# Kernel optimization log

Measured on AMD Instinct MI355X. Metric: run time of the kernel, lower is better.

Reference implementation:

```python
import jax, jax.numpy as jnp
import numpy as np

B, S, D = 8, 2048, 512
EPS = 1e-6
ROPE_THETA = 10000.0


def setup_inputs() -> dict:
    key = jax.random.key(0)
    ks = jax.random.split(key, 8)
    scale = 0.02
    return {
        "x": jax.random.normal(ks[0], (B, S, D), dtype=jnp.float32),
        "conv_w": jax.random.normal(ks[1], (D, D, 3), dtype=jnp.float32) * scale,
        "conv_b": jnp.zeros((D,), dtype=jnp.float32),
        "pre_g": jnp.ones((D,), dtype=jnp.float32),
        "q_g": jnp.ones((D,), dtype=jnp.float32),
        "k_g": jnp.ones((D,), dtype=jnp.float32),
        "Wq": jax.random.normal(ks[2], (D, D), dtype=jnp.float32) * scale,
        "Wk": jax.random.normal(ks[3], (D, D), dtype=jnp.float32) * scale,
        "Wv": jax.random.normal(ks[4], (D, D), dtype=jnp.float32) * scale,
    }


def _rmsnorm(x, g, eps=EPS):
    ms = jnp.mean(jnp.square(x), axis=-1, keepdims=True)
    return x * jax.lax.rsqrt(ms + eps) * g


def _rope_tables(seq_len, head_dim, dtype=jnp.float32):
    inv = 1.0 / (ROPE_THETA ** (jnp.arange(0, head_dim, 2, dtype=dtype) / head_dim))
    freqs = jnp.arange(seq_len, dtype=dtype)[:, None] * inv[None, :]  # [S, D/2]
    return jnp.cos(freqs), jnp.sin(freqs)


def _apply_rope(x, cos, sin):
    # x: [B, S, D]; treat last dim as D/2 complex pairs (interleaved real/imag)
    b, s, d = x.shape
    xr = x.reshape(b, s, d // 2, 2)
    x0, x1 = xr[..., 0], xr[..., 1]
    c = cos[None, :, :]
    sn = sin[None, :, :]
    o0 = x0 * c - x1 * sn
    o1 = x0 * sn + x1 * c
    return jnp.stack([o0, o1], axis=-1).reshape(b, s, d)


def reference(x, conv_w, conv_b, pre_g, q_g, k_g, Wq, Wk, Wv):
    b, s, d = x.shape
    # Conv1d over sequence axis (kernel 3, padding 1)
    xc = jnp.transpose(x, (0, 2, 1))  # [B, D, S]
    xc = jax.lax.conv_general_dilated(
        xc, conv_w, window_strides=(1,), padding=[(1, 1)],
        dimension_numbers=("NCH", "OIH", "NCH"))
    xc = xc + conv_b[None, :, None]
    x_norm = _rmsnorm(jnp.transpose(xc, (0, 2, 1)), pre_g)  # [B, S, D]

    q = _rmsnorm(jnp.einsum("bsd,ed->bse", x_norm, Wq), q_g)
    k = _rmsnorm(jnp.einsum("bsd,ed->bse", x_norm, Wk), k_g)
    v = jnp.einsum("bsd,ed->bse", x_norm, Wv)

    cos, sin = _rope_tables(s, d, x.dtype)
    q = _apply_rope(q, cos, sin)
    k = _apply_rope(k, cos, sin)

    scores = jnp.einsum("bqd,bkd->bqk", q, k) / jnp.sqrt(jnp.asarray(d, x.dtype))
    w = jax.nn.softmax(scores, axis=-1)  # dropout is identity in eval mode
    attended = jnp.einsum("bqk,bkd->bqd", w, v)
    out = x + attended
    return out.mean(axis=1)  # [B, D]
```

## Files before the change

### kernel.cpp

```cpp
#include <hip/hip_runtime.h>
#include <math.h>

#define BB 8
#define SS 2048
#define DDIM 512
#define KC 1536
#define EPSV 1e-6f
#define SCALE 0.044194173824159216f
#define LDP 40

typedef unsigned short ushort_t;
using short8 = __attribute__((ext_vector_type(8))) short;
using f32x4  = __attribute__((ext_vector_type(4))) float;

__device__ inline unsigned short f2bf(float f) {
    union { float f; unsigned int u; } v; v.f = f;
    unsigned int r = v.u + 0x7FFFu + ((v.u >> 16) & 1u);
    return (unsigned short)(r >> 16);
}
__device__ inline unsigned int packbf(float a, float b) {
    return (unsigned int)f2bf(a) | ((unsigned int)f2bf(b) << 16);
}
__device__ inline float bf2f(unsigned short s) {
    union { unsigned int u; float f; } v; v.u = ((unsigned int)s) << 16; return v.f;
}
__device__ inline short8 ldfrag(const ushort_t* s, int row, int ko) {
    return *reinterpret_cast<const short8*>(&s[row * LDP + ko]);
}

__global__ __launch_bounds__(256) void kx_cast(const float* __restrict__ x, ushort_t* __restrict__ xbf)
{
    int i = (blockIdx.x * 256 + threadIdx.x) * 4;
    float4 v = *reinterpret_cast<const float4*>(&x[i]);
    unsigned int lo = packbf(v.x, v.y), hi = packbf(v.z, v.w);
    *reinterpret_cast<uint2*>(&xbf[i]) = make_uint2(lo, hi);
}

__global__ __launch_bounds__(256) void k0_prep(
    const float* __restrict__ conv_w, const float* __restrict__ Wq,
    const float* __restrict__ Wk, const float* __restrict__ Wv,
    ushort_t* __restrict__ wcat, ushort_t* __restrict__ wqkv)
{
    int idx = blockIdx.x * 256 + threadIdx.x;
    {
        int o = idx / KC, kk = idx - o * KC;
        int t = kk >> 9, i = kk & 511;
        wcat[idx] = f2bf(conv_w[(size_t)o * KC + i * 3 + t]);
    }
    {
        int n = idx >> 9, d = idx & 511;
        const float* src = (n < 512) ? &Wq[(size_t)n * DDIM + d]
                         : (n < 1024) ? &Wk[(size_t)(n - 512) * DDIM + d]
                         : &Wv[(size_t)(n - 1024) * DDIM + d];
        wqkv[idx] = f2bf(*src);
    }
}

__global__ __launch_bounds__(256, 4) void k1b_conv(
    const ushort_t* __restrict__ xbf, const ushort_t* __restrict__ wcat,
    const float* __restrict__ conv_b, float* __restrict__ y, float* __restrict__ rs)
{
    __shared__ ushort_t As[128 * LDP];
    __shared__ ushort_t Bs[128 * LDP];
    const int t = threadIdx.x;
    const int lane = t & 63, w = t >> 6;
    const int lm = lane & 15, lq = lane >> 4;
    const int wm = w >> 1, wn = w & 1;
    const int srow = t >> 2, scol = (t & 3) * 8;
    const int s0 = blockIdx.x * 128;
    const int n0 = blockIdx.y * 128;
    const int b  = blockIdx.z;
    const ushort_t* Ag = xbf + (size_t)b * SS * DDIM;
    const ushort_t* Bg = wcat + (size_t)n0 * KC;

    f32x4 acc[4][4];
    #pragma unroll
    for (int i = 0; i < 4; i++)
        #pragma unroll
        for (int j = 0; j < 4; j++) acc[i][j] = (f32x4){0.f, 0.f, 0.f, 0.f};

    const uint4 z4 = make_uint4(0, 0, 0, 0);
    #define LOADA(dc, ro, dst) { \
        int s_ = s0 + srow + (ro) + ((dc) >> 4) - 1; \
        int ic_ = (((dc) & 15) << 5) + scol; \
        dst = (s_ >= 0 && s_ < SS) ? *reinterpret_cast<const uint4*>(&Ag[(size_t)s_ * DDIM + ic_]) : z4; }

    uint4 ra0, ra1, rb0, rb1;
    LOADA(0, 0, ra0); LOADA(0, 64, ra1);
    rb0 = *reinterpret_cast<const uint4*>(&Bg[(size_t)srow * KC + scol]);
    rb1 = *reinterpret_cast<const uint4*>(&Bg[(size_t)(srow + 64) * KC + scol]);

    for (int dc = 0; dc < 48; dc++) {
        *reinterpret_cast<uint4*>(&As[srow * LDP + scol]) = ra0;
        *reinterpret_cast<uint4*>(&As[(srow + 64) * LDP + scol]) = ra1;
        *reinterpret_cast<uint4*>(&Bs[srow * LDP + scol]) = rb0;
        *reinterpret_cast<uint4*>(&Bs[(srow + 64) * LDP + scol]) = rb1;
        __syncthreads();
        if (dc < 47) {
            LOADA(dc + 1, 0, ra0); LOADA(dc + 1, 64, ra1);
            int c = (dc + 1) * 32 + scol;
            rb0 = *reinterpret_cast<const uint4*>(&Bg[(size_t)srow * KC + c]);
            rb1 = *reinterpret_cast<const uint4*>(&Bg[(size_t)(srow + 64) * KC + c]);
        }
        short8 af[4];
        #pragma unroll
        for (int mt = 0; mt < 4; mt++)
            af[mt] = ldfrag(As, wm * 64 + mt * 16 + lm, lq * 8);
        #pragma unroll
        for (int nt = 0; nt < 4; nt++) {
            short8 bfv = ldfrag(Bs, wn * 64 + nt * 16 + lm, lq * 8);
            #pragma unroll
            for (int mt = 0; mt < 4; mt++)
                acc[mt][nt] = __builtin_amdgcn_mfma_f32_16x16x32_bf16(af[mt], bfv, acc[mt][nt], 0, 0, 0);
        }
        __syncthreads();
    }
    #undef LOADA

    const int rbase = s0 + wm * 64;
    const int cbase = n0 + wn * 64;
    float* yb  = y + (size_t)b * SS * DDIM;
    float* rsb = rs + (size_t)b * SS;
    float bias[4];
    #pragma unroll
    for (int nt = 0; nt < 4; nt++) bias[nt] = conv_b[cbase + nt * 16 + lm];
    #pragma unroll
    for (int mt = 0; mt < 4; mt++) {
        float pr[4] = {0.f, 0.f, 0.f, 0.f};
        #pragma unroll
        for (int nt = 0; nt < 4; nt++) {
            #pragma unroll
            for (int r = 0; r < 4; r++) {
                float val = acc[mt][nt][r] + bias[nt];
                yb[(size_t)(rbase + mt * 16 + lq * 4 + r) * DDIM + cbase + nt * 16 + lm] = val;
                pr[r] = fmaf(val, val, pr[r]);
            }
        }
        #pragma unroll
        for (int r = 0; r < 4; r++) {
            float p = pr[r];
            p += __shfl_xor(p, 1, 64); p += __shfl_xor(p, 2, 64);
            p += __shfl_xor(p, 4, 64); p += __shfl_xor(p, 8, 64);
            if (lm == 0) atomicAdd(&rsb[rbase + mt * 16 + lq * 4 + r], p);
        }
    }
}

__global__ __launch_bounds__(256) void k1n_norm(
    const float* __restrict__ y, const float* __restrict__ rs,
    const float* __restrict__ pre_g, ushort_t* __restrict__ xnbf)
{
    const int t = threadIdx.x;
    const int b = blockIdx.y;
    const int r0 = blockIdx.x * 8;
    float2 pg = *reinterpret_cast<const float2*>(&pre_g[2 * t]);
    for (int r = 0; r < 8; r++) {
        size_t row = (size_t)b * SS + r0 + r;
        float inv = rsqrtf(rs[row] * (1.0f / DDIM) + EPSV);
        float2 v = *reinterpret_cast<const float2*>(&y[row * DDIM + 2 * t]);
        *reinterpret_cast<unsigned int*>(&xnbf[row * DDIM + 2 * t]) =
            packbf(v.x * inv * pg.x, v.y * inv * pg.y);
    }
}

__global__ __launch_bounds__(256, 4) void k1c_qkv(
    const ushort_t* __restrict__ xnbf, const ushort_t* __restrict__ wqkv,
    float* __restrict__ qraw, float* __restrict__ kraw, ushort_t* __restrict__ vb,
    float* __restrict__ rq, float* __restrict__ rk)
{
    __shared__ ushort_t As[128 * LDP];
    __shared__ ushort_t Bs[128 * LDP];
    const int t = threadIdx.x;
    const int lane = t & 63, w = t >> 6;
    const int lm = lane & 15, lq = lane >> 4;
    const int wm = w >> 1, wn = w & 1;
    const int srow = t >> 2, scol = (t & 3) * 8;
    const int s0 = blockIdx.x * 128;
    const int n0 = blockIdx.y * 128;
    const int b  = blockIdx.z;
    const ushort_t* Ag = xnbf + (size_t)b * SS * DDIM;
    const ushort_t* Bg = wqkv + (size_t)n0 * DDIM;

    f32x4 acc[4][4];
    #pragma unroll
    for (int i = 0; i < 4; i++)
        #pragma unroll
        for (int j = 0; j < 4; j++) acc[i][j] = (f32x4){0.f, 0.f, 0.f, 0.f};

    uint4 ra0 = *reinterpret_cast<const uint4*>(&Ag[(size_t)(s0 + srow) * DDIM + scol]);
    uint4 ra1 = *reinterpret_cast<const uint4*>(&Ag[(size_t)(s0 + srow + 64) * DDIM + scol]);
    uint4 rb0 = *reinterpret_cast<const uint4*>(&Bg[(size_t)srow * DDIM + scol]);
    uint4 rb1 = *reinterpret_cast<const uint4*>(&Bg[(size_t)(srow + 64) * DDIM + scol]);

    for (int dc = 0; dc < 16; dc++) {
        *reinterpret_cast<uint4*>(&As[srow * LDP + scol]) = ra0;
        *reinterpret_cast<uint4*>(&As[(srow + 64) * LDP + scol]) = ra1;
        *reinterpret_cast<uint4*>(&Bs[srow * LDP + scol]) = rb0;
        *reinterpret_cast<uint4*>(&Bs[(srow + 64) * LDP + scol]) = rb1;
        __syncthreads();
        if (dc < 15) {
            int c = (dc + 1) * 32 + scol;
            ra0 = *reinterpret_cast<const uint4*>(&Ag[(size_t)(s0 + srow) * DDIM + c]);
            ra1 = *reinterpret_cast<const uint4*>(&Ag[(size_t)(s0 + srow + 64) * DDIM + c]);
            rb0 = *reinterpret_cast<const uint4*>(&Bg[(size_t)srow * DDIM + c]);
            rb1 = *reinterpret_cast<const uint4*>(&Bg[(size_t)(srow + 64) * DDIM + c]);
        }
        short8 af[4];
        #pragma unroll
        for (int mt = 0; mt < 4; mt++)
            af[mt] = ldfrag(As, wm * 64 + mt * 16 + lm, lq * 8);
        #pragma unroll
        for (int nt = 0; nt < 4; nt++) {
            short8 bfv = ldfrag(Bs, wn * 64 + nt * 16 + lm, lq * 8);
            #pragma unroll
            for (int mt = 0; mt < 4; mt++)
                acc[mt][nt] = __builtin_amdgcn_mfma_f32_16x16x32_bf16(af[mt], bfv, acc[mt][nt], 0, 0, 0);
        }
        __syncthreads();
    }

    const int which = blockIdx.y >> 2;
    const int rbase = s0 + wm * 64;
    const int cbase = ((blockIdx.y & 3) * 128) + wn * 64;
    if (which == 2) {
        ushort_t* vbb = vb + (size_t)b * SS * DDIM;
        #pragma unroll
        for (int mt = 0; mt < 4; mt++)
            #pragma unroll
            for (int nt = 0; nt < 4; nt++)
                #pragma unroll
                for (int r = 0; r < 4; r++)
                    vbb[(size_t)(rbase + mt * 16 + lq * 4 + r) * DDIM + cbase + nt * 16 + lm] =
                        f2bf(acc[mt][nt][r]);
    } else {
        float* dst = which ? kraw : qraw;
        float* rr  = which ? rk : rq;
        float* db  = dst + (size_t)b * SS * DDIM;
        float* rb  = rr + (size_t)b * SS;
        #pragma unroll
        for (int mt = 0; mt < 4; mt++) {
            float pr[4] = {0.f, 0.f, 0.f, 0.f};
            #pragma unroll
            for (int nt = 0; nt < 4; nt++) {
                #pragma unroll
                for (int r = 0; r < 4; r++) {
                    float val = acc[mt][nt][r];
                    db[(size_t)(rbase + mt * 16 + lq * 4 + r) * DDIM + cbase + nt * 16 + lm] = val;
                    pr[r] = fmaf(val, val, pr[r]);
                }
            }
            #pragma unroll
            for (int r = 0; r < 4; r++) {
                float p = pr[r];
                p += __shfl_xor(p, 1, 64); p += __shfl_xor(p, 2, 64);
                p += __shfl_xor(p, 4, 64); p += __shfl_xor(p, 8, 64);
                if (lm == 0) atomicAdd(&rb[rbase + mt * 16 + lq * 4 + r], p);
            }
        }
    }
}

__global__ __launch_bounds__(256) void k1d_rope(
    const float* __restrict__ qraw, const float* __restrict__ kraw,
    const float* __restrict__ rq, const float* __restrict__ rk,
    const float* __restrict__ q_g, const float* __restrict__ k_g,
    ushort_t* __restrict__ qb, ushort_t* __restrict__ kb)
{
    const int t = threadIdx.x;
    const int b = blockIdx.y;
    const int r0 = blockIdx.x * 8;
    const int c0 = 2 * t;
    float qg0 = q_g[c0], qg1 = q_g[c0 + 1];
    float kg0 = k_g[c0], kg1 = k_g[c0 + 1];
    float invf = (float)pow(10000.0, -(double)c0 / (double)DDIM);
    for (int r = 0; r < 8; r++) {
        int srow = r0 + r;
        size_t rowi = (size_t)b * SS + srow;
        float iq = rsqrtf(rq[rowi] * (1.0f / DDIM) + EPSV);
        float ik = rsqrtf(rk[rowi] * (1.0f / DDIM) + EPSV);
        size_t off = rowi * DDIM + c0;
        float2 qv = *reinterpret_cast<const float2*>(&qraw[off]);
        float2 kv = *reinterpret_cast<const float2*>(&kraw[off]);
        float q0 = qv.x * iq * qg0, q1 = qv.y * iq * qg1;
        float k0v = kv.x * ik * kg0, k1v = kv.y * ik * kg1;
        float ang = (float)srow * invf, sn, cs;
        sincosf(ang, &sn, &cs);
        *reinterpret_cast<unsigned int*>(&qb[off]) = packbf(q0 * cs - q1 * sn, q0 * sn + q1 * cs);
        *reinterpret_cast<unsigned int*>(&kb[off]) = packbf(k0v * cs - k1v * sn, k0v * sn + k1v * cs);
    }
}

__global__ __launch_bounds__(256, 4) void k2a_rowsum(
    const ushort_t* __restrict__ qb, const ushort_t* __restrict__ kb,
    ushort_t* __restrict__ P, float* __restrict__ l)
{
    __shared__ ushort_t As[128 * LDP];
    __shared__ ushort_t Bs[128 * LDP];
    const int t = threadIdx.x;
    const int lane = t & 63, w = t >> 6;
    const int lm = lane & 15, lq = lane >> 4;
    const int wm = w >> 1, wn = w & 1;
    const int srow = t >> 2, scol = (t & 3) * 8;

    const ushort_t* Ag = qb + ((size_t)blockIdx.z * SS + blockIdx.x * 128) * DDIM;
    const ushort_t* Bg = kb + ((size_t)blockIdx.z * SS + blockIdx.y * 128) * DDIM;

    f32x4 acc[4][4];
    #pragma unroll
    for (int i = 0; i < 4; i++)
        #pragma unroll
        for (int j = 0; j < 4; j++) acc[i][j] = (f32x4){0.f, 0.f, 0.f, 0.f};

    uint4 ra0 = *reinterpret_cast<const uint4*>(&Ag[(size_t)srow * DDIM + scol]);
    uint4 ra1 = *reinterpret_cast<const uint4*>(&Ag[(size_t)(srow + 64) * DDIM + scol]);
    uint4 rb0 = *reinterpret_cast<const uint4*>(&Bg[(size_t)srow * DDIM + scol]);
    uint4 rb1 = *reinterpret_cast<const uint4*>(&Bg[(size_t)(srow + 64) * DDIM + scol]);

    for (int dc = 0; dc < 16; dc++) {
        *reinterpret_cast<uint4*>(&As[srow * LDP + scol]) = ra0;
        *reinterpret_cast<uint4*>(&As[(srow + 64) * LDP + scol]) = ra1;
        *reinterpret_cast<uint4*>(&Bs[srow * LDP + scol]) = rb0;
        *reinterpret_cast<uint4*>(&Bs[(srow + 64) * LDP + scol]) = rb1;
        __syncthreads();
        if (dc < 15) {
            int off = (dc + 1) * 32 + scol;
            ra0 = *reinterpret_cast<const uint4*>(&Ag[(size_t)srow * DDIM + off]);
            ra1 = *reinterpret_cast<const uint4*>(&Ag[(size_t)(srow + 64) * DDIM + off]);
            rb0 = *reinterpret_cast<const uint4*>(&Bg[(size_t)srow * DDIM + off]);
            rb1 = *reinterpret_cast<const uint4*>(&Bg[(size_t)(srow + 64) * DDIM + off]);
        }
        short8 af[4];
        #pragma unroll
        for (int mt = 0; mt < 4; mt++)
            af[mt] = ldfrag(As, wm * 64 + mt * 16 + lm, lq * 8);
        #pragma unroll
        for (int nt = 0; nt < 4; nt++) {
            short8 bfv = ldfrag(Bs, wn * 64 + nt * 16 + lm, lq * 8);
            #pragma unroll
            for (int mt = 0; mt < 4; mt++)
                acc[mt][nt] = __builtin_amdgcn_mfma_f32_16x16x32_bf16(af[mt], bfv, acc[mt][nt], 0, 0, 0);
        }
        __syncthreads();
    }

    const int rbase = blockIdx.x * 128 + wm * 64;
    const int cbase = blockIdx.y * 128 + wn * 64;
    ushort_t* Pb = P + (size_t)blockIdx.z * SS * SS;
    float* lrow = l + (size_t)blockIdx.z * SS;
    #pragma unroll
    for (int mt = 0; mt < 4; mt++) {
        #pragma unroll
        for (int r = 0; r < 4; r++) {
            const int row = rbase + mt * 16 + lq * 4 + r;
            float rowp = 0.f;
            #pragma unroll
            for (int nt = 0; nt < 4; nt++) {
                float e = __expf(acc[mt][nt][r] * SCALE);
                Pb[(size_t)row * SS + cbase + nt * 16 + lm] = f2bf(e);
                rowp += e;
            }
            float p = rowp;
            p += __shfl_xor(p, 1, 64); p += __shfl_xor(p, 2, 64);
            p += __shfl_xor(p, 4, 64); p += __shfl_xor(p, 8, 64);
            if (lm == 0) atomicAdd(&lrow[row], p);
        }
    }
}

__global__ __launch_bounds__(256) void k2c_colred(
    const ushort_t* __restrict__ P, const float* __restrict__ l,
    float* __restrict__ cw)
{
    const int t = threadIdx.x;
    const int b = blockIdx.z;
    const int k0 = blockIdx.x * 512 + t * 2;
    const int q0 = blockIdx.y * 128;
    const ushort_t* Pb = P + ((size_t)b * SS + q0) * SS;
    const float* lb = l + (size_t)b * SS + q0;
    float a0 = 0.f, a1 = 0.f;
    for (int q = 0; q < 128; q++) {
        float rl = 1.0f / lb[q];
        unsigned int pp = *reinterpret_cast<const unsigned int*>(&Pb[(size_t)q * SS + k0]);
        a0 = fmaf(bf2f((ushort_t)(pp & 0xFFFF)), rl, a0);
        a1 = fmaf(bf2f((ushort_t)(pp >> 16)), rl, a1);
    }
    atomicAdd(&cw[(size_t)b * SS + k0], a0);
    atomicAdd(&cw[(size_t)b * SS + k0 + 1], a1);
}

__global__ __launch_bounds__(256) void k4_out(
    const float* __restrict__ x, const ushort_t* __restrict__ v,
    const float* __restrict__ cwv, float* __restrict__ out)
{
    const int b = blockIdx.x, c = blockIdx.y;
    const int t = threadIdx.x;
    const int srow0 = c * (SS / 16);
    const float* xb    = x + ((size_t)b * SS + srow0) * DDIM;
    const ushort_t* vb = v + ((size_t)b * SS + srow0) * DDIM;
    const float* cwb   = cwv + (size_t)b * SS + srow0;
    float a0 = 0.f, a1 = 0.f;
    for (int r = 0; r < SS / 16; r++) {
        float w = cwb[r];
        a0 += xb[(size_t)r * DDIM + t]       + w * bf2f(vb[(size_t)r * DDIM + t]);
        a1 += xb[(size_t)r * DDIM + t + 256] + w * bf2f(vb[(size_t)r * DDIM + t + 256]);
    }
    atomicAdd(&out[b * DDIM + t],       a0 * (1.0f / SS));
    atomicAdd(&out[b * DDIM + t + 256], a1 * (1.0f / SS));
}

extern "C" void kernel_launch(void* const* d_in, const int* in_sizes, int n_in,
                              void* d_out, int out_size, void* d_ws, size_t ws_size,
                              hipStream_t stream)
{
    const float* x      = (const float*)d_in[0];
    const float* conv_w = (const float*)d_in[1];
    const float* conv_b = (const float*)d_in[2];
    const float* pre_g  = (const float*)d_in[3];
    const float* q_g    = (const float*)d_in[4];
    const float* k_g    = (const float*)d_in[5];
    const float* Wq     = (const float*)d_in[6];
    const float* Wk     = (const float*)d_in[7];
    const float* Wv     = (const float*)d_in[8];
    float* out          = (float*)d_out;

    const size_t NTOK = (size_t)BB * SS * DDIM;
    char* p = (char*)d_ws;
    float* y_qraw  = (float*)p; p += NTOK * 4;
    float* kraw    = (float*)p; p += NTOK * 4;
    ushort_t* xbf_vb = (ushort_t*)p; p += NTOK * 2;
    ushort_t* xn_qb  = (ushort_t*)p; p += NTOK * 2;
    ushort_t* kb     = (ushort_t*)p; p += NTOK * 2;
    ushort_t* wcat   = (ushort_t*)p; p += (size_t)DDIM * KC * 2;
    ushort_t* wqkv   = (ushort_t*)p; p += (size_t)KC * DDIM * 2;
    float* rs   = (float*)p; p += (size_t)BB * SS * 4;
    float* rq   = (float*)p; p += (size_t)BB * SS * 4;
    float* rk   = (float*)p; p += (size_t)BB * SS * 4;
    float* lbuf = (float*)p; p += (size_t)BB * SS * 4;
    float* cwb  = (float*)p; p += (size_t)BB * SS * 4;

    ushort_t* Pbuf = (ushort_t*)y_qraw;

    (void)hipMemsetAsync(d_out, 0, (size_t)out_size * sizeof(float), stream);
    (void)hipMemsetAsync(rs, 0, (size_t)BB * SS * 5 * sizeof(float), stream);

    kx_cast<<<dim3((unsigned)(NTOK / 1024)), 256, 0, stream>>>(x, xbf_vb);
    k0_prep<<<dim3(DDIM * KC / 256), 256, 0, stream>>>(conv_w, Wq, Wk, Wv, wcat, wqkv);
    k1b_conv<<<dim3(SS / 128, 4, BB), 256, 0, stream>>>(xbf_vb, wcat, conv_b, y_qraw, rs);
    k1n_norm<<<dim3(SS / 8, BB), 256, 0, stream>>>(y_qraw, rs, pre_g, xn_qb);
    k1c_qkv<<<dim3(SS / 128, 12, BB), 256, 0, stream>>>(xn_qb, wqkv, y_qraw, kraw, xbf_vb, rq, rk);
    k1d_rope<<<dim3(SS / 8, BB), 256, 0, stream>>>(y_qraw, kraw, rq, rk, q_g, k_g, xn_qb, kb);
    k2a_rowsum<<<dim3(SS / 128, SS / 128, BB), 256, 0, stream>>>(xn_qb, kb, Pbuf, lbuf);
    k2c_colred<<<dim3(SS / 512, SS / 128, BB), 256, 0, stream>>>(Pbuf, lbuf, cwb);
    k4_out<<<dim3(BB, 16), 256, 0, stream>>>(x, xbf_vb, cwb, out);
}
```

Before: 295.9 us.

## Store conv and QK intermediates as bf16, reorder score grid, widen column reduction

```diff
diff --git a/kernel.cpp b/kernel.cpp
--- a/kernel.cpp
+++ b/kernel.cpp
@@ -58,7 +58,7 @@
 
 __global__ __launch_bounds__(256, 4) void k1b_conv(
     const ushort_t* __restrict__ xbf, const ushort_t* __restrict__ wcat,
-    const float* __restrict__ conv_b, float* __restrict__ y, float* __restrict__ rs)
+    const float* __restrict__ conv_b, ushort_t* __restrict__ ybf, float* __restrict__ rs)
 {
     __shared__ ushort_t As[128 * LDP];
     __shared__ ushort_t Bs[128 * LDP];
@@ -119,7 +119,7 @@
 
     const int rbase = s0 + wm * 64;
     const int cbase = n0 + wn * 64;
-    float* yb  = y + (size_t)b * SS * DDIM;
+    ushort_t* yb = ybf + (size_t)b * SS * DDIM;
     float* rsb = rs + (size_t)b * SS;
     float bias[4];
     #pragma unroll
@@ -132,7 +132,7 @@
             #pragma unroll
             for (int r = 0; r < 4; r++) {
                 float val = acc[mt][nt][r] + bias[nt];
-                yb[(size_t)(rbase + mt * 16 + lq * 4 + r) * DDIM + cbase + nt * 16 + lm] = val;
+                yb[(size_t)(rbase + mt * 16 + lq * 4 + r) * DDIM + cbase + nt * 16 + lm] = f2bf(val);
                 pr[r] = fmaf(val, val, pr[r]);
             }
         }
@@ -147,7 +147,7 @@
 }
 
 __global__ __launch_bounds__(256) void k1n_norm(
-    const float* __restrict__ y, const float* __restrict__ rs,
+    const ushort_t* __restrict__ ybf, const float* __restrict__ rs,
     const float* __restrict__ pre_g, ushort_t* __restrict__ xnbf)
 {
     const int t = threadIdx.x;
@@ -157,15 +157,16 @@
     for (int r = 0; r < 8; r++) {
         size_t row = (size_t)b * SS + r0 + r;
         float inv = rsqrtf(rs[row] * (1.0f / DDIM) + EPSV);
-        float2 v = *reinterpret_cast<const float2*>(&y[row * DDIM + 2 * t]);
+        unsigned int yv = *reinterpret_cast<const unsigned int*>(&ybf[row * DDIM + 2 * t]);
+        float v0 = bf2f((ushort_t)(yv & 0xFFFF)), v1 = bf2f((ushort_t)(yv >> 16));
         *reinterpret_cast<unsigned int*>(&xnbf[row * DDIM + 2 * t]) =
-            packbf(v.x * inv * pg.x, v.y * inv * pg.y);
+            packbf(v0 * inv * pg.x, v1 * inv * pg.y);
     }
 }
 
 __global__ __launch_bounds__(256, 4) void k1c_qkv(
     const ushort_t* __restrict__ xnbf, const ushort_t* __restrict__ wqkv,
-    float* __restrict__ qraw, float* __restrict__ kraw, ushort_t* __restrict__ vb,
+    ushort_t* __restrict__ qraw, ushort_t* __restrict__ kraw, ushort_t* __restrict__ vb,
     float* __restrict__ rq, float* __restrict__ rk)
 {
     __shared__ ushort_t As[128 * LDP];
@@ -233,10 +234,8 @@
                     vbb[(size_t)(rbase + mt * 16 + lq * 4 + r) * DDIM + cbase + nt * 16 + lm] =
                         f2bf(acc[mt][nt][r]);
     } else {
-        float* dst = which ? kraw : qraw;
-        float* rr  = which ? rk : rq;
-        float* db  = dst + (size_t)b * SS * DDIM;
-        float* rb  = rr + (size_t)b * SS;
+        ushort_t* db = (which ? kraw : qraw) + (size_t)b * SS * DDIM;
+        float* rb = (which ? rk : rq) + (size_t)b * SS;
         #pragma unroll
         for (int mt = 0; mt < 4; mt++) {
             float pr[4] = {0.f, 0.f, 0.f, 0.f};
@@ -245,7 +244,7 @@
                 #pragma unroll
                 for (int r = 0; r < 4; r++) {
                     float val = acc[mt][nt][r];
-                    db[(size_t)(rbase + mt * 16 + lq * 4 + r) * DDIM + cbase + nt * 16 + lm] = val;
+                    db[(size_t)(rbase + mt * 16 + lq * 4 + r) * DDIM + cbase + nt * 16 + lm] = f2bf(val);
                     pr[r] = fmaf(val, val, pr[r]);
                 }
             }
@@ -261,10 +260,9 @@
 }
 
 __global__ __launch_bounds__(256) void k1d_rope(
-    const float* __restrict__ qraw, const float* __restrict__ kraw,
+    ushort_t* q_io, ushort_t* k_io,
     const float* __restrict__ rq, const float* __restrict__ rk,
-    const float* __restrict__ q_g, const float* __restrict__ k_g,
-    ushort_t* __restrict__ qb, ushort_t* __restrict__ kb)
+    const float* __restrict__ q_g, const float* __restrict__ k_g)
 {
     const int t = threadIdx.x;
     const int b = blockIdx.y;
@@ -279,14 +277,16 @@
         float iq = rsqrtf(rq[rowi] * (1.0f / DDIM) + EPSV);
         float ik = rsqrtf(rk[rowi] * (1.0f / DDIM) + EPSV);
         size_t off = rowi * DDIM + c0;
-        float2 qv = *reinterpret_cast<const float2*>(&qraw[off]);
-        float2 kv = *reinterpret_cast<const float2*>(&kraw[off]);
-        float q0 = qv.x * iq * qg0, q1 = qv.y * iq * qg1;
-        float k0v = kv.x * ik * kg0, k1v = kv.y * ik * kg1;
+        unsigned int qv = *reinterpret_cast<const unsigned int*>(&q_io[off]);
+        unsigned int kv = *reinterpret_cast<const unsigned int*>(&k_io[off]);
+        float q0 = bf2f((ushort_t)(qv & 0xFFFF)) * iq * qg0;
+        float q1 = bf2f((ushort_t)(qv >> 16)) * iq * qg1;
+        float k0v = bf2f((ushort_t)(kv & 0xFFFF)) * ik * kg0;
+        float k1v = bf2f((ushort_t)(kv >> 16)) * ik * kg1;
         float ang = (float)srow * invf, sn, cs;
         sincosf(ang, &sn, &cs);
-        *reinterpret_cast<unsigned int*>(&qb[off]) = packbf(q0 * cs - q1 * sn, q0 * sn + q1 * cs);
-        *reinterpret_cast<unsigned int*>(&kb[off]) = packbf(k0v * cs - k1v * sn, k0v * sn + k1v * cs);
+        *reinterpret_cast<unsigned int*>(&q_io[off]) = packbf(q0 * cs - q1 * sn, q0 * sn + q1 * cs);
+        *reinterpret_cast<unsigned int*>(&k_io[off]) = packbf(k0v * cs - k1v * sn, k0v * sn + k1v * cs);
     }
 }
 
@@ -301,9 +301,12 @@
     const int lm = lane & 15, lq = lane >> 4;
     const int wm = w >> 1, wn = w & 1;
     const int srow = t >> 2, scol = (t & 3) * 8;
-
-    const ushort_t* Ag = qb + ((size_t)blockIdx.z * SS + blockIdx.x * 128) * DDIM;
-    const ushort_t* Bg = kb + ((size_t)blockIdx.z * SS + blockIdx.y * 128) * DDIM;
+    const int b  = blockIdx.x;
+    const int qt = blockIdx.y;
+    const int kt = blockIdx.z;
+
+    const ushort_t* Ag = qb + ((size_t)b * SS + qt * 128) * DDIM;
+    const ushort_t* Bg = kb + ((size_t)b * SS + kt * 128) * DDIM;
 
     f32x4 acc[4][4];
     #pragma unroll
@@ -343,10 +346,10 @@
         __syncthreads();
     }
 
-    const int rbase = blockIdx.x * 128 + wm * 64;
-    const int cbase = blockIdx.y * 128 + wn * 64;
-    ushort_t* Pb = P + (size_t)blockIdx.z * SS * SS;
-    float* lrow = l + (size_t)blockIdx.z * SS;
+    const int rbase = qt * 128 + wm * 64;
+    const int cbase = kt * 128 + wn * 64;
+    ushort_t* Pb = P + (size_t)b * SS * SS;
+    float* lrow = l + (size_t)b * SS;
     #pragma unroll
     for (int mt = 0; mt < 4; mt++) {
         #pragma unroll
@@ -373,19 +376,23 @@
 {
     const int t = threadIdx.x;
     const int b = blockIdx.z;
-    const int k0 = blockIdx.x * 512 + t * 2;
+    const int k0 = blockIdx.x * 1024 + t * 4;
     const int q0 = blockIdx.y * 128;
     const ushort_t* Pb = P + ((size_t)b * SS + q0) * SS;
     const float* lb = l + (size_t)b * SS + q0;
-    float a0 = 0.f, a1 = 0.f;
+    float a0 = 0.f, a1 = 0.f, a2 = 0.f, a3 = 0.f;
     for (int q = 0; q < 128; q++) {
         float rl = 1.0f / lb[q];
-        unsigned int pp = *reinterpret_cast<const unsigned int*>(&Pb[(size_t)q * SS + k0]);
-        a0 = fmaf(bf2f((ushort_t)(pp & 0xFFFF)), rl, a0);
-        a1 = fmaf(bf2f((ushort_t)(pp >> 16)), rl, a1);
+        uint2 pp = *reinterpret_cast<const uint2*>(&Pb[(size_t)q * SS + k0]);
+        a0 = fmaf(bf2f((ushort_t)(pp.x & 0xFFFF)), rl, a0);
+        a1 = fmaf(bf2f((ushort_t)(pp.x >> 16)), rl, a1);
+        a2 = fmaf(bf2f((ushort_t)(pp.y & 0xFFFF)), rl, a2);
+        a3 = fmaf(bf2f((ushort_t)(pp.y >> 16)), rl, a3);
     }
     atomicAdd(&cw[(size_t)b * SS + k0], a0);
     atomicAdd(&cw[(size_t)b * SS + k0 + 1], a1);
+    atomicAdd(&cw[(size_t)b * SS + k0 + 2], a2);
+    atomicAdd(&cw[(size_t)b * SS + k0 + 3], a3);
 }
 
 __global__ __launch_bounds__(256) void k4_out(
@@ -425,31 +432,33 @@
 
     const size_t NTOK = (size_t)BB * SS * DDIM;
     char* p = (char*)d_ws;
-    float* y_qraw  = (float*)p; p += NTOK * 4;
-    float* kraw    = (float*)p; p += NTOK * 4;
-    ushort_t* xbf_vb = (ushort_t*)p; p += NTOK * 2;
-    ushort_t* xn_qb  = (ushort_t*)p; p += NTOK * 2;
-    ushort_t* kb     = (ushort_t*)p; p += NTOK * 2;
-    ushort_t* wcat   = (ushort_t*)p; p += (size_t)DDIM * KC * 2;
-    ushort_t* wqkv   = (ushort_t*)p; p += (size_t)KC * DDIM * 2;
+    ushort_t* xbf = (ushort_t*)p; p += NTOK * 2;
+    ushort_t* ybf = (ushort_t*)p; p += NTOK * 2;
+    ushort_t* xn  = (ushort_t*)p; p += NTOK * 2;
+                         p += NTOK * 2;
+    ushort_t* qio = (ushort_t*)p; p += NTOK * 2;
+    ushort_t* kio = (ushort_t*)p; p += NTOK * 2;
+    ushort_t* vb  = (ushort_t*)p; p += NTOK * 2;
+    ushort_t* wcat = (ushort_t*)p; p += (size_t)DDIM * KC * 2;
+    ushort_t* wqkv = (ushort_t*)p; p += (size_t)KC * DDIM * 2;
     float* rs   = (float*)p; p += (size_t)BB * SS * 4;
     float* rq   = (float*)p; p += (size_t)BB * SS * 4;
     float* rk   = (float*)p; p += (size_t)BB * SS * 4;
     float* lbuf = (float*)p; p += (size_t)BB * SS * 4;
     float* cwb  = (float*)p; p += (size_t)BB * SS * 4;
 
-    ushort_t* Pbuf = (ushort_t*)y_qraw;
+    ushort_t* Pbuf = xbf;
 
     (void)hipMemsetAsync(d_out, 0, (size_t)out_size * sizeof(float), stream);
     (void)hipMemsetAsync(rs, 0, (size_t)BB * SS * 5 * sizeof(float), stream);
 
-    kx_cast<<<dim3((unsigned)(NTOK / 1024)), 256, 0, stream>>>(x, xbf_vb);
+    kx_cast<<<dim3((unsigned)(NTOK / 1024)), 256, 0, stream>>>(x, xbf);
     k0_prep<<<dim3(DDIM * KC / 256), 256, 0, stream>>>(conv_w, Wq, Wk, Wv, wcat, wqkv);
-    k1b_conv<<<dim3(SS / 128, 4, BB), 256, 0, stream>>>(xbf_vb, wcat, conv_b, y_qraw, rs);
-    k1n_norm<<<dim3(SS / 8, BB), 256, 0, stream>>>(y_qraw, rs, pre_g, xn_qb);
-    k1c_qkv<<<dim3(SS / 128, 12, BB), 256, 0, stream>>>(xn_qb, wqkv, y_qraw, kraw, xbf_vb, rq, rk);
-    k1d_rope<<<dim3(SS / 8, BB), 256, 0, stream>>>(y_qraw, kraw, rq, rk, q_g, k_g, xn_qb, kb);
-    k2a_rowsum<<<dim3(SS / 128, SS / 128, BB), 256, 0, stream>>>(xn_qb, kb, Pbuf, lbuf);
-    k2c_colred<<<dim3(SS / 512, SS / 128, BB), 256, 0, stream>>>(Pbuf, lbuf, cwb);
-    k4_out<<<dim3(BB, 16), 256, 0, stream>>>(x, xbf_vb, cwb, out);
-}
+    k1b_conv<<<dim3(SS / 128, 4, BB), 256, 0, stream>>>(xbf, wcat, conv_b, ybf, rs);
+    k1n_norm<<<dim3(SS / 8, BB), 256, 0, stream>>>(ybf, rs, pre_g, xn);
+    k1c_qkv<<<dim3(SS / 128, 12, BB), 256, 0, stream>>>(xn, wqkv, qio, kio, vb, rq, rk);
+    k1d_rope<<<dim3(SS / 8, BB), 256, 0, stream>>>(qio, kio, rq, rk, q_g, k_g);
+    k2a_rowsum<<<dim3(BB, SS / 128, SS / 128), 256, 0, stream>>>(qio, kio, Pbuf, lbuf);
+    k2c_colred<<<dim3(SS / 1024, SS / 128, BB), 256, 0, stream>>>(Pbuf, lbuf, cwb);
+    k4_out<<<dim3(BB, 16), 256, 0, stream>>>(x, vb, cwb, out);
+}
```

Result: faster. 287.8 us (-2.8%).
